# Kernel optimization log

Measured on AMD Instinct MI355X. Metric: run time of the kernel, lower is better.

Reference implementation:

```python
import jax, jax.numpy as jnp
import numpy as np

N, F, H, C = 2048, 64, 64, 8

def setup_inputs() -> dict:
    key = jax.random.key(0)
    ks = jax.random.split(key, 8)
    s = 0.05  # small init like xavier gain=0.01
    return {
        "x": jax.random.normal(ks[0], (N, F), jnp.float32),
        "node_distances": jax.random.uniform(ks[1], (N, N), jnp.float32),
        "normalization_matrix": jnp.ones((N, N), jnp.float32),
        "W1": jax.random.normal(ks[2], (F, H), jnp.float32) * s,
        "b1": jnp.zeros((F, H), jnp.float32),
        "W2": jax.random.normal(ks[3], (F, H, C), jnp.float32) * s,
        "b2": jnp.zeros((F, C), jnp.float32),
        "Wm1": jax.random.normal(ks[4], (H,), jnp.float32) * s,
        "bm1": jnp.zeros((H,), jnp.float32),
        "Wm2": jax.random.normal(ks[5], (H,), jnp.float32) * s,
        "bm2": jnp.zeros((), jnp.float32),
    }

def reference(x, node_distances, normalization_matrix, W1, b1, W2, b2, Wm1, bm1, Wm2, bm2):
    # Per-feature NAM MLPs, vectorized over all F features (input dim is 1).
    # h[n,f,:] = relu(x[n,f] * W1[f] + b1[f])
    h = jax.nn.relu(x[:, :, None] * W1[None, :, :] + b1[None, :, :])        # [N,F,H]
    fx = jnp.einsum('nfh,fhc->nfc', h, W2) + b2[None, :, :]                 # [N,F,C]
    # Distance MLP m: Linear(1,H)->ReLU->Linear(H,1), limited_m => scalar weight per pair.
    d = node_distances / normalization_matrix                               # [N,N]
    hm = jax.nn.relu(d[:, :, None] * Wm1 + bm1)                             # [N,N,H]
    m = hm @ Wm2 + bm2                                                      # [N,N]
    # mf[c,i,f] = sum_j m[i,j]*fx[j,f,c]; out[c,i] = sum_f mf[c,i,f]
    # => out[i,c] = sum_j m[i,j] * (sum_f fx[j,f,c])  (identical math, fused)
    g = fx.sum(axis=1)                                                      # [N,C]
    out = m @ g                                                             # [N,C] == torch out.T
    return out
```

## Files before the change

kernel.cpp:

```cpp
#include <hip/hip_runtime.h>

#define NN 2048
#define FF 64
#define HH 64
#define CC 8
#define NB 2
#define JPT 8

__global__ __launch_bounds__(256) void g_kernel(
    const float* __restrict__ x, const float* __restrict__ W1,
    const float* __restrict__ b1, const float* __restrict__ W2,
    const float* __restrict__ b2, float* __restrict__ g)
{
    const int wave = (blockIdx.x * 256 + threadIdx.x) >> 6;
    const int lane = threadIdx.x & 63;
    const int n0 = wave * NB;

    float xr[NB];
#pragma unroll
    for (int j = 0; j < NB; ++j) xr[j] = x[(n0 + j) * FF + lane];

    float acc[NB][CC];
#pragma unroll
    for (int j = 0; j < NB; ++j)
#pragma unroll
        for (int c = 0; c < CC; ++c) acc[j][c] = 0.f;

    float bs[CC];
    {
        const float4* bp = (const float4*)&b2[lane * CC];
        float4 a = bp[0], b = bp[1];
        bs[0] = a.x; bs[1] = a.y; bs[2] = a.z; bs[3] = a.w;
        bs[4] = b.x; bs[5] = b.y; bs[6] = b.z; bs[7] = b.w;
    }

#pragma unroll 4
    for (int f = 0; f < FF; ++f) {
        float w1 = W1[f * HH + lane];
        float bb = b1[f * HH + lane];
        const float4* w2p = (const float4*)&W2[(f * HH + lane) * CC];
        float4 wa = w2p[0];
        float4 wb = w2p[1];
#pragma unroll
        for (int j = 0; j < NB; ++j) {
            float xv = __shfl(xr[j], f);
            float hv = fmaxf(fmaf(xv, w1, bb), 0.f);
            acc[j][0] = fmaf(hv, wa.x, acc[j][0]);
            acc[j][1] = fmaf(hv, wa.y, acc[j][1]);
            acc[j][2] = fmaf(hv, wa.z, acc[j][2]);
            acc[j][3] = fmaf(hv, wa.w, acc[j][3]);
            acc[j][4] = fmaf(hv, wb.x, acc[j][4]);
            acc[j][5] = fmaf(hv, wb.y, acc[j][5]);
            acc[j][6] = fmaf(hv, wb.z, acc[j][6]);
            acc[j][7] = fmaf(hv, wb.w, acc[j][7]);
        }
    }

#pragma unroll
    for (int s = 32; s >= 1; s >>= 1) {
#pragma unroll
        for (int j = 0; j < NB; ++j)
#pragma unroll
            for (int c = 0; c < CC; ++c)
                acc[j][c] += __shfl_xor(acc[j][c], s);
#pragma unroll
        for (int c = 0; c < CC; ++c)
            bs[c] += __shfl_xor(bs[c], s);
    }

    if (lane == 0) {
#pragma unroll
        for (int j = 0; j < NB; ++j)
#pragma unroll
            for (int c = 0; c < CC; ++c)
                g[(n0 + j) * CC + c] = acc[j][c] + bs[c];
    }
}

__global__ __launch_bounds__(256) void out_kernel(
    const float* __restrict__ nd, const float* __restrict__ nm,
    const float* __restrict__ Wm1, const float* __restrict__ bm1,
    const float* __restrict__ Wm2, const float* __restrict__ bm2,
    const float* __restrict__ g, float* __restrict__ out)
{
    const int i = blockIdx.x;
    const int t = threadIdx.x;
    const float bm2v = bm2[0];

    float dv[JPT];
#pragma unroll
    for (int jj = 0; jj < JPT; ++jj) {
        int j = jj * 256 + t;
        dv[jj] = nd[i * NN + j] / nm[i * NN + j];
    }

    float m[JPT];
#pragma unroll
    for (int jj = 0; jj < JPT; ++jj) m[jj] = bm2v;

#pragma unroll 8
    for (int h = 0; h < HH; ++h) {
        float w1 = Wm1[h];
        float bb = bm1[h];
        float w2 = Wm2[h];
#pragma unroll
        for (int jj = 0; jj < JPT; ++jj) {
            float hv = fmaxf(fmaf(dv[jj], w1, bb), 0.f);
            m[jj] = fmaf(hv, w2, m[jj]);
        }
    }

    float acc[CC];
#pragma unroll
    for (int c = 0; c < CC; ++c) acc[c] = 0.f;

#pragma unroll
    for (int jj = 0; jj < JPT; ++jj) {
        int j = jj * 256 + t;
        const float4* gp = (const float4*)&g[j * CC];
        float4 ga = gp[0];
        float4 gb = gp[1];
        acc[0] = fmaf(m[jj], ga.x, acc[0]);
        acc[1] = fmaf(m[jj], ga.y, acc[1]);
        acc[2] = fmaf(m[jj], ga.z, acc[2]);
        acc[3] = fmaf(m[jj], ga.w, acc[3]);
        acc[4] = fmaf(m[jj], gb.x, acc[4]);
        acc[5] = fmaf(m[jj], gb.y, acc[5]);
        acc[6] = fmaf(m[jj], gb.z, acc[6]);
        acc[7] = fmaf(m[jj], gb.w, acc[7]);
    }

#pragma unroll
    for (int s = 32; s >= 1; s >>= 1) {
#pragma unroll
        for (int c = 0; c < CC; ++c)
            acc[c] += __shfl_xor(acc[c], s);
    }

    __shared__ float red[4][CC];
    const int wv = t >> 6;
    const int lane = t & 63;
    if (lane == 0) {
#pragma unroll
        for (int c = 0; c < CC; ++c) red[wv][c] = acc[c];
    }
    __syncthreads();
    if (t < CC) {
        out[i * CC + t] = red[0][t] + red[1][t] + red[2][t] + red[3][t];
    }
}

extern "C" void kernel_launch(void* const* d_in, const int* in_sizes, int n_in,
                              void* d_out, int out_size, void* d_ws, size_t ws_size,
                              hipStream_t stream) {
    const float* x   = (const float*)d_in[0];
    const float* nd  = (const float*)d_in[1];
    const float* nm  = (const float*)d_in[2];
    const float* W1  = (const float*)d_in[3];
    const float* b1  = (const float*)d_in[4];
    const float* W2  = (const float*)d_in[5];
    const float* b2  = (const float*)d_in[6];
    const float* Wm1 = (const float*)d_in[7];
    const float* bm1 = (const float*)d_in[8];
    const float* Wm2 = (const float*)d_in[9];
    const float* bm2 = (const float*)d_in[10];
    float* out = (float*)d_out;
    float* g   = (float*)d_ws;

    g_kernel<<<NN / (NB * 4), 256, 0, stream>>>(x, W1, b1, W2, b2, g);
    out_kernel<<<NN, 256, 0, stream>>>(nd, nm, Wm1, bm1, Wm2, bm2, g, out);
}
```

Measured before the change: 135.4 us.

## Replace per-pair distance MLP with piecewise-linear lookup via sorted ReLU breakpoints

The scalar distance MLP is a sum of ReLUs, so it is piecewise linear in d. A new prep kernel sorts the 64 breakpoints -b/w with a bitonic sort and precomputes a slope and intercept for each of the 65 intervals. Each (i,j) pair in the main kernel then costs a binary search in shared memory and one FMA, instead of 64 FMA+max+FMA steps. The diff also switches the nd/nm loads to float4 and replaces the division with a refined reciprocal, which changes the j-to-thread mapping and adds one more launch plus LDS lookups that may bank-conflict.

Result: slower. 146.2 us (+8.0%).

```diff
diff --git a/kernel.cpp b/kernel.cpp
--- a/kernel.cpp
+++ b/kernel.cpp
@@ -5,7 +5,71 @@
 #define HH 64
 #define CC 8
 #define NB 2
-#define JPT 8
+
+#define INF __builtin_inff()
+
+#define WS_T 0
+#define WS_A 64
+#define WS_B 129
+#define WS_G 256
+
+__global__ __launch_bounds__(64) void prep_kernel(
+    const float* __restrict__ Wm1, const float* __restrict__ bm1,
+    const float* __restrict__ Wm2, const float* __restrict__ bm2,
+    float* __restrict__ ws)
+{
+    const int lane = threadIdx.x;
+    __shared__ float lw[HH], lb[HH], lm2[HH], lt[HH], ls[HH];
+
+    float w = Wm1[lane];
+    float b = bm1[lane];
+    float m2 = Wm2[lane];
+    float t = (w != 0.f) ? (-b / w) : INF;
+    lw[lane] = w; lb[lane] = b; lm2[lane] = m2; lt[lane] = t;
+
+    float v = t;
+#pragma unroll
+    for (int k = 2; k <= 64; k <<= 1) {
+#pragma unroll
+        for (int j = k >> 1; j >= 1; j >>= 1) {
+            float o = __shfl_xor(v, j);
+            bool up = ((lane & k) == 0);
+            bool lower = ((lane & j) == 0);
+            float mn = fminf(v, o), mx = fmaxf(v, o);
+            v = (up == lower) ? mn : mx;
+        }
+    }
+    ls[lane] = v;
+    ws[WS_T + lane] = v;
+    __syncthreads();
+
+    const float bm2v = bm2[0];
+    for (int k = lane; k < 65; k += 64) {
+        float lo = (k == 0) ? -INF : ls[k - 1];
+        float hi = (k == 64) ? INF : ls[k];
+        float dt;
+        if (k == 0) {
+            dt = (hi == INF) ? 0.f : hi - 1.f;
+        } else if (hi == INF) {
+            dt = (lo == INF) ? INF : lo + 1.f;
+        } else {
+            dt = 0.5f * (lo + hi);
+        }
+        float alpha = 0.f, beta = bm2v;
+#pragma unroll 8
+        for (int h = 0; h < HH; ++h) {
+            float wh = lw[h], bh = lb[h], mh = lm2[h], th = lt[h];
+            bool act = (wh > 0.f) ? (dt > th)
+                     : ((wh < 0.f) ? (dt < th) : (bh > 0.f));
+            if (act) {
+                alpha = fmaf(mh, wh, alpha);
+                beta  = fmaf(mh, bh, beta);
+            }
+        }
+        ws[WS_A + k] = alpha;
+        ws[WS_B + k] = beta;
+    }
+}
 
 __global__ __launch_bounds__(256) void g_kernel(
     const float* __restrict__ x, const float* __restrict__ W1,
@@ -79,34 +143,32 @@
 
 __global__ __launch_bounds__(256) void out_kernel(
     const float* __restrict__ nd, const float* __restrict__ nm,
-    const float* __restrict__ Wm1, const float* __restrict__ bm1,
-    const float* __restrict__ Wm2, const float* __restrict__ bm2,
-    const float* __restrict__ g, float* __restrict__ out)
+    const float* __restrict__ ws, const float* __restrict__ g,
+    float* __restrict__ out)
 {
     const int i = blockIdx.x;
     const int t = threadIdx.x;
-    const float bm2v = bm2[0];
-
-    float dv[JPT];
-#pragma unroll
-    for (int jj = 0; jj < JPT; ++jj) {
-        int j = jj * 256 + t;
-        dv[jj] = nd[i * NN + j] / nm[i * NN + j];
-    }
-
-    float m[JPT];
-#pragma unroll
-    for (int jj = 0; jj < JPT; ++jj) m[jj] = bm2v;
-
-#pragma unroll 8
-    for (int h = 0; h < HH; ++h) {
-        float w1 = Wm1[h];
-        float bb = bm1[h];
-        float w2 = Wm2[h];
-#pragma unroll
-        for (int jj = 0; jj < JPT; ++jj) {
-            float hv = fmaxf(fmaf(dv[jj], w1, bb), 0.f);
-            m[jj] = fmaf(hv, w2, m[jj]);
+
+    __shared__ float Tl[64], Al[65], Bl[65];
+    if (t < 64) Tl[t] = ws[WS_T + t];
+    else if (t < 129) Al[t - 64] = ws[WS_A + (t - 64)];
+    else if (t < 194) Bl[t - 129] = ws[WS_B + (t - 129)];
+    __syncthreads();
+
+    const float4* nd4 = (const float4*)(nd + (size_t)i * NN);
+    const float4* nm4 = (const float4*)(nm + (size_t)i * NN);
+    float dv[8];
+#pragma unroll
+    for (int p = 0; p < 2; ++p) {
+        float4 a = nd4[p * 256 + t];
+        float4 b = nm4[p * 256 + t];
+        float na[4] = {a.x, a.y, a.z, a.w};
+        float nb[4] = {b.x, b.y, b.z, b.w};
+#pragma unroll
+        for (int e = 0; e < 4; ++e) {
+            float r = __builtin_amdgcn_rcpf(nb[e]);
+            r = r * fmaf(-nb[e], r, 2.0f);
+            dv[p * 4 + e] = na[e] * r;
         }
     }
 
@@ -115,19 +177,30 @@
     for (int c = 0; c < CC; ++c) acc[c] = 0.f;
 
 #pragma unroll
-    for (int jj = 0; jj < JPT; ++jj) {
-        int j = jj * 256 + t;
-        const float4* gp = (const float4*)&g[j * CC];
-        float4 ga = gp[0];
-        float4 gb = gp[1];
-        acc[0] = fmaf(m[jj], ga.x, acc[0]);
-        acc[1] = fmaf(m[jj], ga.y, acc[1]);
-        acc[2] = fmaf(m[jj], ga.z, acc[2]);
-        acc[3] = fmaf(m[jj], ga.w, acc[3]);
-        acc[4] = fmaf(m[jj], gb.x, acc[4]);
-        acc[5] = fmaf(m[jj], gb.y, acc[5]);
-        acc[6] = fmaf(m[jj], gb.z, acc[6]);
-        acc[7] = fmaf(m[jj], gb.w, acc[7]);
+    for (int p = 0; p < 2; ++p) {
+#pragma unroll
+        for (int e = 0; e < 4; ++e) {
+            float d = dv[p * 4 + e];
+            int lo = 0;
+#pragma unroll
+            for (int s = 32; s >= 1; s >>= 1)
+                lo += (Tl[lo + s - 1] < d) ? s : 0;
+            lo += (Tl[lo] < d) ? 1 : 0;
+            float m = fmaf(d, Al[lo], Bl[lo]);
+
+            int j = p * 1024 + t * 4 + e;
+            const float4* gp = (const float4*)&g[j * CC];
+            float4 ga = gp[0];
+            float4 gb = gp[1];
+            acc[0] = fmaf(m, ga.x, acc[0]);
+            acc[1] = fmaf(m, ga.y, acc[1]);
+            acc[2] = fmaf(m, ga.z, acc[2]);
+            acc[3] = fmaf(m, ga.w, acc[3]);
+            acc[4] = fmaf(m, gb.x, acc[4]);
+            acc[5] = fmaf(m, gb.y, acc[5]);
+            acc[6] = fmaf(m, gb.z, acc[6]);
+            acc[7] = fmaf(m, gb.w, acc[7]);
+        }
     }
 
 #pragma unroll
@@ -165,8 +238,9 @@
     const float* Wm2 = (const float*)d_in[9];
     const float* bm2 = (const float*)d_in[10];
     float* out = (float*)d_out;
-    float* g   = (float*)d_ws;
-
-    g_kernel<<<NN / (NB * 4), 256, 0, stream>>>(x, W1, b1, W2, b2, g);
-    out_kernel<<<NN, 256, 0, stream>>>(nd, nm, Wm1, bm1, Wm2, bm2, g, out);
-}
+    float* ws  = (float*)d_ws;
+
+    prep_kernel<<<1, 64, 0, stream>>>(Wm1, bm1, Wm2, bm2, ws);
+    g_kernel<<<NN / (NB * 4), 256, 0, stream>>>(x, W1, b1, W2, b2, ws + WS_G);
+    out_kernel<<<NN, 256, 0, stream>>>(nd, nm, ws, ws + WS_G, out);
+}
```
